# Optimization experiments

Measured on AMD Instinct MI355X. Metric: run time of the kernel, lower is better.

Reference implementation:

```python
import jax, jax.numpy as jnp
import numpy as np

N_EMBD = 1024
N_HEAD = 16
D_K = N_EMBD // N_HEAD


def setup_inputs() -> dict:
    key = jax.random.key(0)
    ks = jax.random.split(key, 9)
    B, L, D = 4, 2048, N_EMBD
    s = 1.0 / np.sqrt(D)
    inp = {
        "x": jax.random.normal(ks[0], (B, L, D), dtype=jnp.float32),
        "mask": jnp.tril(jnp.ones((1, 1, L, L), dtype=jnp.int32)),
        "Wq": jax.random.uniform(ks[1], (D, D), jnp.float32, -s, s),
        "bq": jax.random.uniform(ks[2], (D,), jnp.float32, -s, s),
        "Wk": jax.random.uniform(ks[3], (D, D), jnp.float32, -s, s),
        "bk": jax.random.uniform(ks[4], (D,), jnp.float32, -s, s),
        "Wv": jax.random.uniform(ks[5], (D, D), jnp.float32, -s, s),
        "bv": jax.random.uniform(ks[6], (D,), jnp.float32, -s, s),
        "Wo": jax.random.uniform(ks[7], (D, D), jnp.float32, -s, s),
        "bo": jax.random.uniform(ks[8], (D,), jnp.float32, -s, s),
    }
    return inp


def reference(x, mask, Wq, bq, Wk, bk, Wv, bv, Wo, bo):
    B, L, D = x.shape
    H, dk = N_HEAD, D_K
    # torch nn.Linear: y = x @ W.T + b
    def proj(W, b):
        y = jnp.einsum('bld,ed->ble', x, W) + b
        return y.reshape(B, L, H, dk).transpose(0, 2, 1, 3)  # [B,H,L,dk]
    q = proj(Wq, bq)
    k = proj(Wk, bk)
    v = proj(Wv, bv)
    scores = jnp.einsum('bhqd,bhkd->bhqk', q, k) / jnp.sqrt(jnp.float32(dk))
    scores = jnp.where(mask == 0, -jnp.inf, scores)
    attn_weights = jax.nn.softmax(scores, axis=-1)  # [B,H,L,L]
    out = jnp.einsum('bhqk,bhkd->bhqd', attn_weights, v)
    out = out.transpose(0, 2, 1, 3).reshape(B, L, D)
    out = jnp.einsum('bld,ed->ble', out, Wo) + bo
    return out, attn_weights
```

## Files before the change

### kernel.cpp

```cpp
#include <hip/hip_runtime.h>
#include <stdint.h>


typedef __attribute__((ext_vector_type(8))) __bf16 bf16x8;
typedef __attribute__((ext_vector_type(4))) float f32x4;

__device__ inline unsigned short f2b(float f) {
  union { float f; unsigned int i; } v; v.f = f;
  unsigned int i = v.i;
  return (unsigned short)((i + 0x7fffu + ((i >> 16) & 1u)) >> 16);
}

__device__ inline f32x4 mfma16(bf16x8 a, bf16x8 b, f32x4 c) {
  return __builtin_amdgcn_mfma_f32_16x16x32_bf16(a, b, c, 0, 0, 0);
}

#define GLD16(gp, lp) __builtin_amdgcn_global_load_lds( \
    (const __attribute__((address_space(1))) void*)(gp), \
    (__attribute__((address_space(3))) void*)(lp), 16, 0, 0)

__global__ __launch_bounds__(256) void f2b_kernel(
    const float* __restrict__ src, unsigned short* __restrict__ dst, int n8)
{
  int i = blockIdx.x * 256 + threadIdx.x;
  if (i >= n8) return;
  const float4* s = (const float4*)src;
  float4 a = s[2 * i], b = s[2 * i + 1];
  unsigned short o[8] __attribute__((aligned(16)));
  o[0] = f2b(a.x); o[1] = f2b(a.y); o[2] = f2b(a.z); o[3] = f2b(a.w);
  o[4] = f2b(b.x); o[5] = f2b(b.y); o[6] = f2b(b.z); o[7] = f2b(b.w);
  *(uint4*)(dst + (size_t)i * 8) = *(const uint4*)o;
}

template <bool OUTF32>
__global__ __launch_bounds__(256) void gemm_bt(
    const unsigned short* __restrict__ A, const unsigned short* __restrict__ B,
    const float* __restrict__ bias, void* __restrict__ Cv,
    int M, int N, int K)
{
  __shared__ unsigned short As[128 * 64];
  __shared__ unsigned short Bs[128 * 64];
  const int tid  = threadIdx.x;
  const int w    = tid >> 6;
  const int lane = tid & 63;
  const int ln   = lane & 15;
  const int quad = lane >> 4;
  const int m0 = blockIdx.x * 128;
  const int n0 = blockIdx.y * 128;
  const int wr = (w >> 1) * 64;
  const int wc = (w & 1) * 64;

  f32x4 acc[4][4];
#pragma unroll
  for (int r = 0; r < 4; ++r)
#pragma unroll
    for (int c = 0; c < 4; ++c) acc[r][c] = (f32x4){0.f, 0.f, 0.f, 0.f};

  for (int kb = 0; kb < K; kb += 64) {
#pragma unroll
    for (int i = 0; i < 4; ++i) {
      int ci  = i * 256 + tid;
      int row = ci >> 3;
      int co  = (ci & 7) * 8;
      GLD16(A + (size_t)(m0 + row) * K + kb + co, &As[(i * 256 + w * 64) * 8]);
      GLD16(B + (size_t)(n0 + row) * K + kb + co, &Bs[(i * 256 + w * 64) * 8]);
    }
    __syncthreads();
#pragma unroll
    for (int ks = 0; ks < 2; ++ks) {
      bf16x8 af[4], bfr[4];
#pragma unroll
      for (int r = 0; r < 4; ++r)
        af[r] = *(const bf16x8*)&As[(wr + r * 16 + ln) * 64 + ks * 32 + quad * 8];
#pragma unroll
      for (int c = 0; c < 4; ++c)
        bfr[c] = *(const bf16x8*)&Bs[(wc + c * 16 + ln) * 64 + ks * 32 + quad * 8];
#pragma unroll
      for (int r = 0; r < 4; ++r)
#pragma unroll
        for (int c = 0; c < 4; ++c)
          acc[r][c] = mfma16(af[r], bfr[c], acc[r][c]);
    }
    __syncthreads();
  }
#pragma unroll
  for (int c = 0; c < 4; ++c) {
    int j = n0 + wc + c * 16 + ln;
    float bj = bias[j];
#pragma unroll
    for (int r = 0; r < 4; ++r)
#pragma unroll
      for (int e = 0; e < 4; ++e) {
        int row = m0 + wr + r * 16 + quad * 4 + e;
        float v = acc[r][c][e] + bj;
        if (OUTF32) ((float*)Cv)[(size_t)row * N + j] = v;
        else ((unsigned short*)Cv)[(size_t)row * N + j] = f2b(v);
      }
  }
}

__global__ __launch_bounds__(256) void transpose_v(
    const unsigned short* __restrict__ V, unsigned short* __restrict__ Vt)
{
  __shared__ unsigned short T[64][72];
  const int tid = threadIdx.x;
  const int lt  = blockIdx.x;
  const int bh  = blockIdx.y;
  const int b = bh >> 4, h = bh & 15;
  const int l0 = lt * 64;
#pragma unroll
  for (int i = 0; i < 2; ++i) {
    int ci = i * 256 + tid;
    int row = ci >> 3;
    int co  = (ci & 7) * 8;
    uint4 v = *(const uint4*)(V + (size_t)(b * 2048 + l0 + row) * 1024 + h * 64 + co);
    *(uint4*)&T[row][co] = v;
  }
  __syncthreads();
  const int d   = tid >> 2;
  const int seg = tid & 3;
  unsigned short tmp[16] __attribute__((aligned(16)));
#pragma unroll
  for (int j = 0; j < 16; ++j) tmp[j] = T[seg * 16 + j][d];
  size_t dst = ((size_t)bh * 64 + d) * 2048 + l0 + seg * 16;
  *(uint4*)(Vt + dst)     = *(const uint4*)tmp;
  *(uint4*)(Vt + dst + 8) = *(const uint4*)(tmp + 8);
}

__global__ __launch_bounds__(256) void attn_kernel(
    const unsigned short* __restrict__ Q, const unsigned short* __restrict__ Kg,
    const unsigned short* __restrict__ Vt, float* __restrict__ attnw,
    unsigned short* __restrict__ O)
{
  __shared__ unsigned short Qs[64 * 64];
  __shared__ unsigned short Ks[64 * 64];
  __shared__ unsigned short Vs[64 * 64];
  __shared__ unsigned short Ps[64 * 64];
  const int tid  = threadIdx.x;
  const int w    = tid >> 6;
  const int lane = tid & 63;
  const int ln   = lane & 15;
  const int quad = lane >> 4;
  const int qt = blockIdx.x;
  const int bh = blockIdx.y;
  const int b = bh >> 4, h = bh & 15;
  const int q0 = qt * 64;
  const size_t head_off = (size_t)b * 2048 * 1024 + (size_t)h * 64;

#pragma unroll
  for (int i = 0; i < 2; ++i) {
    int ci = i * 256 + tid;
    int row = ci >> 3;
    int co  = (ci & 7) * 8;
    GLD16(Q + head_off + (size_t)(q0 + row) * 1024 + co, &Qs[(i * 256 + w * 64) * 8]);
  }
  __syncthreads();
  bf16x8 qf0 = *(const bf16x8*)&Qs[(w * 16 + ln) * 64 + quad * 8];
  bf16x8 qf1 = *(const bf16x8*)&Qs[(w * 16 + ln) * 64 + 32 + quad * 8];

  float m[4], l[4];
#pragma unroll
  for (int r = 0; r < 4; ++r) { m[r] = -__builtin_inff(); l[r] = 0.f; }
  const int nkt  = qt + 1;
  const int qrow = q0 + w * 16 + quad * 4;

  for (int kt = 0; kt < nkt; ++kt) {
    __syncthreads();
#pragma unroll
    for (int i = 0; i < 2; ++i) {
      int ci = i * 256 + tid;
      int row = ci >> 3;
      int co  = (ci & 7) * 8;
      GLD16(Kg + head_off + (size_t)(kt * 64 + row) * 1024 + co, &Ks[(i * 256 + w * 64) * 8]);
    }
    __syncthreads();
    float S[4][4];
#pragma unroll
    for (int t = 0; t < 4; ++t) {
      bf16x8 kf0 = *(const bf16x8*)&Ks[(t * 16 + ln) * 64 + quad * 8];
      bf16x8 kf1 = *(const bf16x8*)&Ks[(t * 16 + ln) * 64 + 32 + quad * 8];
      f32x4 s = mfma16(qf0, kf0, (f32x4){0.f, 0.f, 0.f, 0.f});
      s = mfma16(qf1, kf1, s);
      int kidx = kt * 64 + t * 16 + ln;
#pragma unroll
      for (int r = 0; r < 4; ++r)
        S[t][r] = (kidx <= qrow + r) ? s[r] * 0.125f : -__builtin_inff();
    }
#pragma unroll
    for (int r = 0; r < 4; ++r) {
      float v = fmaxf(fmaxf(S[0][r], S[1][r]), fmaxf(S[2][r], S[3][r]));
      v = fmaxf(v, __shfl_xor(v, 1));
      v = fmaxf(v, __shfl_xor(v, 2));
      v = fmaxf(v, __shfl_xor(v, 4));
      v = fmaxf(v, __shfl_xor(v, 8));
      float nm = fmaxf(m[r], v);
      float p = __expf(S[0][r] - nm) + __expf(S[1][r] - nm) +
                __expf(S[2][r] - nm) + __expf(S[3][r] - nm);
      p += __shfl_xor(p, 1);
      p += __shfl_xor(p, 2);
      p += __shfl_xor(p, 4);
      p += __shfl_xor(p, 8);
      l[r] = l[r] * __expf(m[r] - nm) + p;
      m[r] = nm;
    }
  }
  float rl[4];
#pragma unroll
  for (int r = 0; r < 4; ++r) rl[r] = 1.f / l[r];

  f32x4 accO[4];
#pragma unroll
  for (int dt = 0; dt < 4; ++dt) accO[dt] = (f32x4){0.f, 0.f, 0.f, 0.f};

  for (int kt = 0; kt < nkt; ++kt) {
    __syncthreads();
#pragma unroll
    for (int i = 0; i < 2; ++i) {
      int ci = i * 256 + tid;
      int row = ci >> 3;
      int co  = (ci & 7) * 8;
      GLD16(Kg + head_off + (size_t)(kt * 64 + row) * 1024 + co, &Ks[(i * 256 + w * 64) * 8]);
      GLD16(Vt + ((size_t)bh * 64 + row) * 2048 + kt * 64 + co, &Vs[(i * 256 + w * 64) * 8]);
    }
    __syncthreads();
#pragma unroll
    for (int t = 0; t < 4; ++t) {
      bf16x8 kf0 = *(const bf16x8*)&Ks[(t * 16 + ln) * 64 + quad * 8];
      bf16x8 kf1 = *(const bf16x8*)&Ks[(t * 16 + ln) * 64 + 32 + quad * 8];
      f32x4 s = mfma16(qf0, kf0, (f32x4){0.f, 0.f, 0.f, 0.f});
      s = mfma16(qf1, kf1, s);
      int kidx = kt * 64 + t * 16 + ln;
#pragma unroll
      for (int r = 0; r < 4; ++r) {
        float sv = (kidx <= qrow + r) ? s[r] * 0.125f : -__builtin_inff();
        float p  = __expf(sv - m[r]) * rl[r];
        Ps[(w * 16 + quad * 4 + r) * 64 + t * 16 + ln] = f2b(p);
        attnw[((size_t)bh * 2048 + (size_t)(qrow + r)) * 2048 + kt * 64 + t * 16 + ln] = p;
      }
    }
    __threadfence_block();
    bf16x8 pf0 = *(const bf16x8*)&Ps[(w * 16 + ln) * 64 + quad * 8];
    bf16x8 pf1 = *(const bf16x8*)&Ps[(w * 16 + ln) * 64 + 32 + quad * 8];
#pragma unroll
    for (int dt = 0; dt < 4; ++dt) {
      bf16x8 vf0 = *(const bf16x8*)&Vs[(dt * 16 + ln) * 64 + quad * 8];
      bf16x8 vf1 = *(const bf16x8*)&Vs[(dt * 16 + ln) * 64 + 32 + quad * 8];
      accO[dt] = mfma16(pf0, vf0, accO[dt]);
      accO[dt] = mfma16(pf1, vf1, accO[dt]);
    }
  }
  {
    int row = tid >> 2;
    int seg = tid & 3;
    float4 z = make_float4(0.f, 0.f, 0.f, 0.f);
    for (int kt = nkt; kt < 32; ++kt) {
      float* dst = attnw + ((size_t)bh * 2048 + (size_t)(q0 + row)) * 2048 + kt * 64 + seg * 16;
      *(float4*)(dst)      = z;
      *(float4*)(dst + 4)  = z;
      *(float4*)(dst + 8)  = z;
      *(float4*)(dst + 12) = z;
    }
  }
#pragma unroll
  for (int dt = 0; dt < 4; ++dt)
#pragma unroll
    for (int e = 0; e < 4; ++e) {
      int row = w * 16 + quad * 4 + e;
      int col = h * 64 + dt * 16 + ln;
      O[(size_t)(b * 2048 + q0 + row) * 1024 + col] = f2b(accO[dt][e]);
    }
}

extern "C" void kernel_launch(void* const* d_in, const int* in_sizes, int n_in,
                              void* d_out, int out_size, void* d_ws, size_t ws_size,
                              hipStream_t stream) {
  const float* x  = (const float*)d_in[0];
  const float* Wq = (const float*)d_in[2];
  const float* bq = (const float*)d_in[3];
  const float* Wk = (const float*)d_in[4];
  const float* bk = (const float*)d_in[5];
  const float* Wv = (const float*)d_in[6];
  const float* bv = (const float*)d_in[7];
  const float* Wo = (const float*)d_in[8];
  const float* bo = (const float*)d_in[9];

  float* out   = (float*)d_out;
  float* attnw = out + (size_t)8192 * 1024;

  const size_t NE = (size_t)8192 * 1024;
  const size_t WE = (size_t)1024 * 1024;
  unsigned short* xb  = (unsigned short*)d_ws;
  unsigned short* Wqb = xb + NE;
  unsigned short* Wkb = Wqb + WE;
  unsigned short* Wvb = Wkb + WE;
  unsigned short* Wob = Wvb + WE;
  unsigned short* Qb  = Wob + WE;
  unsigned short* Kb  = Qb + NE;
  unsigned short* Vb  = Kb + NE;
  unsigned short* Vtb = xb;
  unsigned short* Ob  = Vb;

  dim3 gb(256);
  f2b_kernel<<<dim3((NE / 8 + 255) / 256), gb, 0, stream>>>(x, xb, (int)(NE / 8));
  f2b_kernel<<<dim3((WE / 8 + 255) / 256), gb, 0, stream>>>(Wq, Wqb, (int)(WE / 8));
  f2b_kernel<<<dim3((WE / 8 + 255) / 256), gb, 0, stream>>>(Wk, Wkb, (int)(WE / 8));
  f2b_kernel<<<dim3((WE / 8 + 255) / 256), gb, 0, stream>>>(Wv, Wvb, (int)(WE / 8));
  f2b_kernel<<<dim3((WE / 8 + 255) / 256), gb, 0, stream>>>(Wo, Wob, (int)(WE / 8));

  dim3 gg(64, 8);
  gemm_bt<false><<<gg, gb, 0, stream>>>(xb, Wqb, bq, Qb, 8192, 1024, 1024);
  gemm_bt<false><<<gg, gb, 0, stream>>>(xb, Wkb, bk, Kb, 8192, 1024, 1024);
  gemm_bt<false><<<gg, gb, 0, stream>>>(xb, Wvb, bv, Vb, 8192, 1024, 1024);
  transpose_v<<<dim3(32, 64), gb, 0, stream>>>(Vb, Vtb);
  attn_kernel<<<dim3(32, 64), gb, 0, stream>>>(Qb, Kb, Vtb, attnw, Ob);
  gemm_bt<true><<<gg, gb, 0, stream>>>(Ob, Wob, bo, out, 8192, 1024, 1024);
}
```

Baseline: 2.111 ms.

## Restructure attention: balanced causal tile pairing, max-free softmax, staged coalesced weight stores

```diff
diff --git a/kernel.cpp b/kernel.cpp
--- a/kernel.cpp
+++ b/kernel.cpp
@@ -18,6 +18,12 @@
 #define GLD16(gp, lp) __builtin_amdgcn_global_load_lds( \
     (const __attribute__((address_space(1))) void*)(gp), \
     (__attribute__((address_space(3))) void*)(lp), 16, 0, 0)
+
+#define VMWAIT(n) asm volatile("s_waitcnt vmcnt(" #n ")" ::: "memory")
+#define LGKM0()   asm volatile("s_waitcnt lgkmcnt(0)" ::: "memory")
+#define BAR()     do { asm volatile("" ::: "memory"); \
+                       __builtin_amdgcn_s_barrier(); \
+                       asm volatile("" ::: "memory"); } while (0)
 
 __global__ __launch_bounds__(256) void f2b_kernel(
     const float* __restrict__ src, unsigned short* __restrict__ dst, int n8)
@@ -127,148 +133,181 @@
   *(uint4*)(Vt + dst + 8) = *(const uint4*)(tmp + 8);
 }
 
-__global__ __launch_bounds__(256) void attn_kernel(
+__device__ __forceinline__ void stage64x64_swz(
+    const unsigned short* __restrict__ g, int gstride,
+    unsigned short* lds, int tid, int w)
+{
+#pragma unroll
+  for (int i = 0; i < 2; ++i) {
+    int ci  = i * 256 + tid;
+    int row = ci >> 3;
+    int c   = (ci & 7) ^ (row & 7);
+    GLD16(g + (size_t)row * gstride + c * 8, lds + (i * 256 + w * 64) * 8);
+  }
+}
+
+__global__ __launch_bounds__(256, 4) void attn_kernel(
     const unsigned short* __restrict__ Q, const unsigned short* __restrict__ Kg,
     const unsigned short* __restrict__ Vt, float* __restrict__ attnw,
     unsigned short* __restrict__ O)
 {
-  __shared__ unsigned short Qs[64 * 64];
-  __shared__ unsigned short Ks[64 * 64];
+  __shared__ unsigned short Ks[2][64 * 64];
   __shared__ unsigned short Vs[64 * 64];
-  __shared__ unsigned short Ps[64 * 64];
+  __shared__ float Psf[64 * 64];
+
   const int tid  = threadIdx.x;
   const int w    = tid >> 6;
   const int lane = tid & 63;
   const int ln   = lane & 15;
   const int quad = lane >> 4;
-  const int qt = blockIdx.x;
   const int bh = blockIdx.y;
   const int b = bh >> 4, h = bh & 15;
-  const int q0 = qt * 64;
   const size_t head_off = (size_t)b * 2048 * 1024 + (size_t)h * 64;
 
-#pragma unroll
-  for (int i = 0; i < 2; ++i) {
-    int ci = i * 256 + tid;
-    int row = ci >> 3;
-    int co  = (ci & 7) * 8;
-    GLD16(Q + head_off + (size_t)(q0 + row) * 1024 + co, &Qs[(i * 256 + w * 64) * 8]);
-  }
-  __syncthreads();
-  bf16x8 qf0 = *(const bf16x8*)&Qs[(w * 16 + ln) * 64 + quad * 8];
-  bf16x8 qf1 = *(const bf16x8*)&Qs[(w * 16 + ln) * 64 + 32 + quad * 8];
-
-  float m[4], l[4];
-#pragma unroll
-  for (int r = 0; r < 4; ++r) { m[r] = -__builtin_inff(); l[r] = 0.f; }
-  const int nkt  = qt + 1;
-  const int qrow = q0 + w * 16 + quad * 4;
-
-  for (int kt = 0; kt < nkt; ++kt) {
-    __syncthreads();
-#pragma unroll
-    for (int i = 0; i < 2; ++i) {
-      int ci = i * 256 + tid;
-      int row = ci >> 3;
-      int co  = (ci & 7) * 8;
-      GLD16(Kg + head_off + (size_t)(kt * 64 + row) * 1024 + co, &Ks[(i * 256 + w * 64) * 8]);
-    }
-    __syncthreads();
-    float S[4][4];
-#pragma unroll
-    for (int t = 0; t < 4; ++t) {
-      bf16x8 kf0 = *(const bf16x8*)&Ks[(t * 16 + ln) * 64 + quad * 8];
-      bf16x8 kf1 = *(const bf16x8*)&Ks[(t * 16 + ln) * 64 + 32 + quad * 8];
-      f32x4 s = mfma16(qf0, kf0, (f32x4){0.f, 0.f, 0.f, 0.f});
-      s = mfma16(qf1, kf1, s);
-      int kidx = kt * 64 + t * 16 + ln;
-#pragma unroll
-      for (int r = 0; r < 4; ++r)
-        S[t][r] = (kidx <= qrow + r) ? s[r] * 0.125f : -__builtin_inff();
-    }
+#pragma unroll 1
+  for (int qi = 0; qi < 2; ++qi) {
+    const int qt   = qi ? (31 - (int)blockIdx.x) : (int)blockIdx.x;
+    const int q0   = qt * 64;
+    const int nkt  = qt + 1;
+    const int qrow = q0 + w * 16 + quad * 4;
+
+    unsigned short* Qst = (unsigned short*)Psf;
+    stage64x64_swz(Q + head_off + (size_t)q0 * 1024, 1024, Qst, tid, w);
+    VMWAIT(0); BAR();
+    bf16x8 qf0, qf1;
+    {
+      int row = w * 16 + ln, r7 = row & 7;
+      qf0 = *(const bf16x8*)&Qst[row * 64 + ((quad    ) ^ r7) * 8];
+      qf1 = *(const bf16x8*)&Qst[row * 64 + (((quad + 4) ^ r7)) * 8];
+    }
+
+    float lsum[4] = {0.f, 0.f, 0.f, 0.f};
+    stage64x64_swz(Kg + head_off, 1024, &Ks[0][0], tid, w);
+    VMWAIT(0); BAR();
+    int cur = 0;
+    for (int kt = 0; kt < nkt; ++kt) {
+      if (kt + 1 < nkt)
+        stage64x64_swz(Kg + head_off + (size_t)(kt + 1) * 64 * 1024, 1024,
+                       &Ks[cur ^ 1][0], tid, w);
+#pragma unroll
+      for (int t = 0; t < 4; ++t) {
+        int row = t * 16 + ln, r7 = row & 7;
+        bf16x8 kf0 = *(const bf16x8*)&Ks[cur][row * 64 + ((quad    ) ^ r7) * 8];
+        bf16x8 kf1 = *(const bf16x8*)&Ks[cur][row * 64 + (((quad + 4) ^ r7)) * 8];
+        f32x4 s = mfma16(qf0, kf0, (f32x4){0.f, 0.f, 0.f, 0.f});
+        s = mfma16(qf1, kf1, s);
+        int kidx = kt * 64 + row;
+#pragma unroll
+        for (int r = 0; r < 4; ++r)
+          lsum[r] += (kidx <= qrow + r) ? __expf(s[r] * 0.125f) : 0.f;
+      }
+      if (kt + 1 < nkt) VMWAIT(0);
+      BAR();
+      cur ^= 1;
+    }
+    float rl[4];
 #pragma unroll
     for (int r = 0; r < 4; ++r) {
-      float v = fmaxf(fmaxf(S[0][r], S[1][r]), fmaxf(S[2][r], S[3][r]));
-      v = fmaxf(v, __shfl_xor(v, 1));
-      v = fmaxf(v, __shfl_xor(v, 2));
-      v = fmaxf(v, __shfl_xor(v, 4));
-      v = fmaxf(v, __shfl_xor(v, 8));
-      float nm = fmaxf(m[r], v);
-      float p = __expf(S[0][r] - nm) + __expf(S[1][r] - nm) +
-                __expf(S[2][r] - nm) + __expf(S[3][r] - nm);
-      p += __shfl_xor(p, 1);
-      p += __shfl_xor(p, 2);
-      p += __shfl_xor(p, 4);
-      p += __shfl_xor(p, 8);
-      l[r] = l[r] * __expf(m[r] - nm) + p;
-      m[r] = nm;
-    }
-  }
-  float rl[4];
-#pragma unroll
-  for (int r = 0; r < 4; ++r) rl[r] = 1.f / l[r];
-
-  f32x4 accO[4];
-#pragma unroll
-  for (int dt = 0; dt < 4; ++dt) accO[dt] = (f32x4){0.f, 0.f, 0.f, 0.f};
-
-  for (int kt = 0; kt < nkt; ++kt) {
-    __syncthreads();
-#pragma unroll
-    for (int i = 0; i < 2; ++i) {
-      int ci = i * 256 + tid;
-      int row = ci >> 3;
-      int co  = (ci & 7) * 8;
-      GLD16(Kg + head_off + (size_t)(kt * 64 + row) * 1024 + co, &Ks[(i * 256 + w * 64) * 8]);
-      GLD16(Vt + ((size_t)bh * 64 + row) * 2048 + kt * 64 + co, &Vs[(i * 256 + w * 64) * 8]);
-    }
-    __syncthreads();
-#pragma unroll
-    for (int t = 0; t < 4; ++t) {
-      bf16x8 kf0 = *(const bf16x8*)&Ks[(t * 16 + ln) * 64 + quad * 8];
-      bf16x8 kf1 = *(const bf16x8*)&Ks[(t * 16 + ln) * 64 + 32 + quad * 8];
-      f32x4 s = mfma16(qf0, kf0, (f32x4){0.f, 0.f, 0.f, 0.f});
-      s = mfma16(qf1, kf1, s);
-      int kidx = kt * 64 + t * 16 + ln;
-#pragma unroll
-      for (int r = 0; r < 4; ++r) {
-        float sv = (kidx <= qrow + r) ? s[r] * 0.125f : -__builtin_inff();
-        float p  = __expf(sv - m[r]) * rl[r];
-        Ps[(w * 16 + quad * 4 + r) * 64 + t * 16 + ln] = f2b(p);
-        attnw[((size_t)bh * 2048 + (size_t)(qrow + r)) * 2048 + kt * 64 + t * 16 + ln] = p;
-      }
-    }
-    __threadfence_block();
-    bf16x8 pf0 = *(const bf16x8*)&Ps[(w * 16 + ln) * 64 + quad * 8];
-    bf16x8 pf1 = *(const bf16x8*)&Ps[(w * 16 + ln) * 64 + 32 + quad * 8];
-#pragma unroll
-    for (int dt = 0; dt < 4; ++dt) {
-      bf16x8 vf0 = *(const bf16x8*)&Vs[(dt * 16 + ln) * 64 + quad * 8];
-      bf16x8 vf1 = *(const bf16x8*)&Vs[(dt * 16 + ln) * 64 + 32 + quad * 8];
-      accO[dt] = mfma16(pf0, vf0, accO[dt]);
-      accO[dt] = mfma16(pf1, vf1, accO[dt]);
-    }
-  }
-  {
-    int row = tid >> 2;
-    int seg = tid & 3;
-    float4 z = make_float4(0.f, 0.f, 0.f, 0.f);
-    for (int kt = nkt; kt < 32; ++kt) {
-      float* dst = attnw + ((size_t)bh * 2048 + (size_t)(q0 + row)) * 2048 + kt * 64 + seg * 16;
-      *(float4*)(dst)      = z;
-      *(float4*)(dst + 4)  = z;
-      *(float4*)(dst + 8)  = z;
-      *(float4*)(dst + 12) = z;
-    }
-  }
-#pragma unroll
-  for (int dt = 0; dt < 4; ++dt)
-#pragma unroll
-    for (int e = 0; e < 4; ++e) {
-      int row = w * 16 + quad * 4 + e;
-      int col = h * 64 + dt * 16 + ln;
-      O[(size_t)(b * 2048 + q0 + row) * 1024 + col] = f2b(accO[dt][e]);
-    }
+      float v = lsum[r];
+      v += __shfl_xor(v, 1); v += __shfl_xor(v, 2);
+      v += __shfl_xor(v, 4); v += __shfl_xor(v, 8);
+      rl[r] = 1.f / v;
+    }
+
+    f32x4 accO[4];
+#pragma unroll
+    for (int dt = 0; dt < 4; ++dt) accO[dt] = (f32x4){0.f, 0.f, 0.f, 0.f};
+    stage64x64_swz(Kg + head_off, 1024, &Ks[0][0], tid, w);
+    VMWAIT(0); BAR();
+    cur = 0;
+    for (int kt = 0; kt < nkt; ++kt) {
+      const int pre = (kt + 1 < nkt);
+      stage64x64_swz(Vt + (size_t)(bh * 64) * 2048 + kt * 64, 2048, Vs, tid, w);
+      if (pre)
+        stage64x64_swz(Kg + head_off + (size_t)(kt + 1) * 64 * 1024, 1024,
+                       &Ks[cur ^ 1][0], tid, w);
+#pragma unroll
+      for (int t = 0; t < 4; ++t) {
+        int row = t * 16 + ln, r7 = row & 7;
+        bf16x8 kf0 = *(const bf16x8*)&Ks[cur][row * 64 + ((quad    ) ^ r7) * 8];
+        bf16x8 kf1 = *(const bf16x8*)&Ks[cur][row * 64 + (((quad + 4) ^ r7)) * 8];
+        f32x4 s = mfma16(qf0, kf0, (f32x4){0.f, 0.f, 0.f, 0.f});
+        s = mfma16(qf1, kf1, s);
+        int kidx = kt * 64 + row;
+#pragma unroll
+        for (int r = 0; r < 4; ++r) {
+          float p = (kidx <= qrow + r) ? __expf(s[r] * 0.125f) * rl[r] : 0.f;
+          int prow = w * 16 + quad * 4 + r;
+          int pc   = t * 16 + ln;
+          Psf[prow * 64 + ((((pc >> 2) ^ (prow & 15)) << 2) | (pc & 3))] = p;
+        }
+      }
+      if (pre) { VMWAIT(2); } else { VMWAIT(0); }
+      LGKM0();
+      BAR();
+      bf16x8 pfr0, pfr1;
+      {
+        int prl = w * 16 + ln, rx = prl & 15;
+        const float* Pr = &Psf[prl * 64];
+        float4 a0 = *(const float4*)&Pr[((2 * quad    ) ^ rx) * 4];
+        float4 a1 = *(const float4*)&Pr[((2 * quad + 1) ^ rx) * 4];
+        float4 b0 = *(const float4*)&Pr[((8 + 2 * quad) ^ rx) * 4];
+        float4 b1 = *(const float4*)&Pr[((9 + 2 * quad) ^ rx) * 4];
+        unsigned short t0[8] __attribute__((aligned(16)));
+        unsigned short t1[8] __attribute__((aligned(16)));
+        t0[0]=f2b(a0.x); t0[1]=f2b(a0.y); t0[2]=f2b(a0.z); t0[3]=f2b(a0.w);
+        t0[4]=f2b(a1.x); t0[5]=f2b(a1.y); t0[6]=f2b(a1.z); t0[7]=f2b(a1.w);
+        t1[0]=f2b(b0.x); t1[1]=f2b(b0.y); t1[2]=f2b(b0.z); t1[3]=f2b(b0.w);
+        t1[4]=f2b(b1.x); t1[5]=f2b(b1.y); t1[6]=f2b(b1.z); t1[7]=f2b(b1.w);
+        pfr0 = *(const bf16x8*)t0;
+        pfr1 = *(const bf16x8*)t1;
+      }
+#pragma unroll
+      for (int dt = 0; dt < 4; ++dt) {
+        int row = dt * 16 + ln, r7 = row & 7;
+        bf16x8 vf0 = *(const bf16x8*)&Vs[row * 64 + ((quad    ) ^ r7) * 8];
+        bf16x8 vf1 = *(const bf16x8*)&Vs[row * 64 + (((quad + 4) ^ r7)) * 8];
+        accO[dt] = mfma16(pfr0, vf0, accO[dt]);
+        accO[dt] = mfma16(pfr1, vf1, accO[dt]);
+      }
+      {
+        int srow = w * 16 + (lane >> 2);
+        int seg  = lane & 3;
+        int rx   = srow & 15;
+        const float* Pr = &Psf[srow * 64];
+        float4 o0 = *(const float4*)&Pr[((4 * seg    ) ^ rx) * 4];
+        float4 o1 = *(const float4*)&Pr[((4 * seg + 1) ^ rx) * 4];
+        float4 o2 = *(const float4*)&Pr[((4 * seg + 2) ^ rx) * 4];
+        float4 o3 = *(const float4*)&Pr[((4 * seg + 3) ^ rx) * 4];
+        float* dst = attnw + ((size_t)bh * 2048 + (size_t)(q0 + srow)) * 2048
+                   + kt * 64 + seg * 16;
+        ((float4*)dst)[0] = o0; ((float4*)dst)[1] = o1;
+        ((float4*)dst)[2] = o2; ((float4*)dst)[3] = o3;
+      }
+      VMWAIT(4);
+      LGKM0();
+      BAR();
+      cur ^= 1;
+    }
+    {
+      int row = tid >> 2, seg = tid & 3;
+      float4 z = make_float4(0.f, 0.f, 0.f, 0.f);
+      for (int kt = nkt; kt < 32; ++kt) {
+        float* dst = attnw + ((size_t)bh * 2048 + (size_t)(q0 + row)) * 2048
+                   + kt * 64 + seg * 16;
+        ((float4*)dst)[0] = z; ((float4*)dst)[1] = z;
+        ((float4*)dst)[2] = z; ((float4*)dst)[3] = z;
+      }
+    }
+#pragma unroll
+    for (int dt = 0; dt < 4; ++dt)
+#pragma unroll
+      for (int e = 0; e < 4; ++e) {
+        int row = w * 16 + quad * 4 + e;
+        int col = h * 64 + dt * 16 + ln;
+        O[(size_t)(b * 2048 + q0 + row) * 1024 + col] = f2b(accO[dt][e]);
+      }
+  }
 }
 
 extern "C" void kernel_launch(void* const* d_in, const int* in_sizes, int n_in,
@@ -312,6 +351,6 @@
   gemm_bt<false><<<gg, gb, 0, stream>>>(xb, Wkb, bk, Kb, 8192, 1024, 1024);
   gemm_bt<false><<<gg, gb, 0, stream>>>(xb, Wvb, bv, Vb, 8192, 1024, 1024);
   transpose_v<<<dim3(32, 64), gb, 0, stream>>>(Vb, Vtb);
-  attn_kernel<<<dim3(32, 64), gb, 0, stream>>>(Qb, Kb, Vtb, attnw, Ob);
+  attn_kernel<<<dim3(16, 64), gb, 0, stream>>>(Qb, Kb, Vtb, attnw, Ob);
   gemm_bt<true><<<gg, gb, 0, stream>>>(Ob, Wob, bo, out, 8192, 1024, 1024);
 }
```

Result: faster. 1.853 ms (-12.2%).
